# Kernel tuning notes

Hardware: AMD Instinct MI355X
Metric: run time of the kernel (lower is better)

The kernel has to match this reference:

```python
import jax, jax.numpy as jnp
import numpy as np

N = 50000       # nodes
E = 1_600_000   # edges (avg degree 32)
IN = 256        # in_dim
HID = 64        # hidden_dim
HEADS = 2
CLS = 10
NEG_SLOPE = 0.2  # PyG GATConv default leaky_relu slope


def gat_layer(x, edge_index, W, att_src, att_dst, bias, heads, concat):
    """PyG-style GATConv (eval mode, add_self_loops=True).
    x: [N, F_in]; W: [F_in, heads*C]; att_src/att_dst: [heads, C]; bias: [heads*C] or [C].
    """
    n = x.shape[0]
    loop = jnp.arange(n)
    src = jnp.concatenate([edge_index[0], loop])   # message sources j
    dst = jnp.concatenate([edge_index[1], loop])   # message targets i
    C = W.shape[1] // heads
    h = (x @ W).reshape(n, heads, C)               # [N, H, C]
    a_s = jnp.sum(h * att_src, axis=-1)            # [N, H]
    a_d = jnp.sum(h * att_dst, axis=-1)            # [N, H]
    e = jax.nn.leaky_relu(a_s[src] + a_d[dst], NEG_SLOPE)   # [E', H]
    # segment softmax over incoming edges of each destination node
    m = jax.lax.stop_gradient(jax.ops.segment_max(e, dst, num_segments=n))
    ex = jnp.exp(e - m[dst])
    denom = jax.ops.segment_sum(ex, dst, num_segments=n)
    alpha = ex / denom[dst]                         # [E', H]
    out = jax.ops.segment_sum(alpha[:, :, None] * h[src], dst, num_segments=n)  # [N, H, C]
    out = out.reshape(n, heads * C) if concat else out.mean(axis=1)
    return out + bias


def setup_inputs() -> dict:
    key = jax.random.key(0)
    ks = jax.random.split(key, 12)
    sd = lambda f: np.float32(1.0 / np.sqrt(f))
    x = jax.random.normal(ks[0], (N, IN), dtype=jnp.float32)
    edge_index = jax.random.randint(ks[1], (2, E), 0, N, dtype=jnp.int64)
    # layer 1: in_dim -> hidden, heads=2, concat
    W1 = jax.random.normal(ks[2], (IN, HEADS * HID), dtype=jnp.float32) * sd(IN)
    as1 = jax.random.normal(ks[3], (HEADS, HID), dtype=jnp.float32) * sd(HID)
    ad1 = jax.random.normal(ks[4], (HEADS, HID), dtype=jnp.float32) * sd(HID)
    b1 = jnp.zeros((HEADS * HID,), dtype=jnp.float32)
    # layer 2: hidden*heads -> hidden, heads=1, concat=False
    W2 = jax.random.normal(ks[5], (HEADS * HID, HID), dtype=jnp.float32) * sd(HEADS * HID)
    as2 = jax.random.normal(ks[6], (1, HID), dtype=jnp.float32) * sd(HID)
    ad2 = jax.random.normal(ks[7], (1, HID), dtype=jnp.float32) * sd(HID)
    b2 = jnp.zeros((HID,), dtype=jnp.float32)
    # linear head
    Wl = jax.random.normal(ks[8], (HID, CLS), dtype=jnp.float32) * sd(HID)
    bl = jnp.zeros((CLS,), dtype=jnp.float32)
    return {"x": x, "edge_index": edge_index,
            "W1": W1, "as1": as1, "ad1": ad1, "b1": b1,
            "W2": W2, "as2": as2, "ad2": ad2, "b2": b2,
            "Wl": Wl, "bl": bl}


def reference(x, edge_index, W1, as1, ad1, b1, W2, as2, ad2, b2, Wl, bl):
    h = jax.nn.elu(gat_layer(x, edge_index, W1, as1, ad1, b1, HEADS, True))
    h = jax.nn.elu(gat_layer(h, edge_index, W2, as2, ad2, b2, 1, False))
    return h @ Wl + bl  # [N, num_classes]
```

## Files before the change

### kernel.cpp

```cpp
#include <hip/hip_runtime.h>

#define NN 50000
#define NE 1600000
#define EP (NE + NN)
#define IN_DIM 256
#define HIDD 64
#define NCLS 10
#define NBKT 196
#define EPB 2048
#define NPB ((EP + EPB - 1) / EPB)
#define BCAP 12288

typedef unsigned short u16;
typedef short bf16x8 __attribute__((ext_vector_type(8)));
typedef float f32x4 __attribute__((ext_vector_type(4)));

__device__ __forceinline__ float b2f(u16 v) { return __uint_as_float(((unsigned)v) << 16); }
__device__ __forceinline__ u16 f2b(float f) {
    unsigned u = __float_as_uint(f);
    unsigned r = (u + 0x7FFFu + ((u >> 16) & 1u)) >> 16;
    return (u16)r;
}

__device__ __forceinline__ void load_edge(const int* __restrict__ ei, int m, int g,
                                          int& s, int& d) {
    if (g < NE) {
        if (m) { s = ei[2 * (size_t)g]; d = ei[2 * ((size_t)NE + g)]; }
        else   { s = ei[g];             d = ei[NE + g]; }
    } else {
        s = d = g - NE;
    }
    s = s < 0 ? 0 : (s >= NN ? NN - 1 : s);
    d = d < 0 ? 0 : (d >= NN ? NN - 1 : d);
}

__device__ __forceinline__ void wcvt_att_job(
    const float* __restrict__ W, const float* __restrict__ as,
    const float* __restrict__ ad, int K, int N, int H, u16* __restrict__ Wt,
    int idx) {
    if (idx >= K * (N + 16)) return;
    int n = idx / K, k = idx - n * K;
    if (n < N) { Wt[idx] = f2b(W[(size_t)k * N + n]); return; }
    int j = n - N;
    if (j >= 2 * H) { Wt[idx] = 0; return; }
    const float* att = (j & 1) ? ad : as;
    int h = j >> 1, C = N / H;
    float sum = 0.f;
    for (int c = 0; c < C; ++c)
        sum += W[(size_t)k * N + h * C + c] * att[h * C + c];
    Wt[idx] = f2b(sum);
}

__global__ __launch_bounds__(256) void wcvt_k(
    const float* __restrict__ W1, const float* __restrict__ as1,
    const float* __restrict__ ad1, u16* __restrict__ w1t,
    const float* __restrict__ W2, const float* __restrict__ as2,
    const float* __restrict__ ad2, u16* __restrict__ w2t,
    const float* __restrict__ Wl, u16* __restrict__ wlt,
    int* __restrict__ gcursor) {
    int b = blockIdx.x, t = threadIdx.x;
    if (b < 144) wcvt_att_job(W1, as1, ad1, 256, 128, 2, w1t, b * 256 + t);
    else if (b < 184) wcvt_att_job(W2, as2, ad2, 128, 64, 1, w2t, (b - 144) * 256 + t);
    else if (b < 188) {
        int idx = (b - 184) * 256 + t;
        int n = idx >> 6, k = idx & 63;
        wlt[n * 64 + k] = (n < NCLS) ? f2b(Wl[k * NCLS + n]) : (u16)0;
    } else {
        if (t < NBKT) gcursor[t] = 0;
    }
}

__device__ void partition_body(int b, const int* __restrict__ ei,
                               int* __restrict__ gcursor,
                               unsigned* __restrict__ bbuf) {
    __shared__ int hist[NBKT], base[NBKT], lbase[NBKT], lcur[NBKT];
    __shared__ int psc[256];
    __shared__ unsigned sst[EPB];
    __shared__ int smode;
    int t = threadIdx.x;
    if (t < 64) {
        int nz = 0;
#pragma unroll
        for (int k = 0; k < 4; ++k)
            if (ei[2 * (t * 4 + k) + 1] != 0) nz = 1;
        unsigned long long bal = __ballot(nz);
        if (t == 0) smode = (bal == 0ULL) ? 1 : 0;
    }
    for (int i = t; i < NBKT; i += 256) hist[i] = 0;
    __syncthreads();
    int m = smode;
    int g0 = b * EPB, gend = min(g0 + EPB, EP);
    unsigned ed[8];
#pragma unroll
    for (int i = 0; i < 4; ++i) {
        int g = g0 + i * 512 + 2 * t;
        int s0 = 0, d0 = 0, s1 = 0, d1 = 0;
        bool v0 = g < gend, v1 = g + 1 < gend;
        if (v1 && g >= NE) {
            s0 = d0 = g - NE; s1 = d1 = g + 1 - NE;
        } else if (v1 && g + 1 < NE) {
            if (m) {
                int4 sv = *(const int4*)(ei + 2 * (size_t)g);
                int4 dv = *(const int4*)(ei + 2 * ((size_t)NE + g));
                s0 = sv.x; s1 = sv.z; d0 = dv.x; d1 = dv.z;
            } else {
                int2 sv = *(const int2*)(ei + g);
                int2 dv = *(const int2*)(ei + NE + g);
                s0 = sv.x; s1 = sv.y; d0 = dv.x; d1 = dv.y;
            }
            s0 = s0 < 0 ? 0 : (s0 >= NN ? NN - 1 : s0);
            d0 = d0 < 0 ? 0 : (d0 >= NN ? NN - 1 : d0);
            s1 = s1 < 0 ? 0 : (s1 >= NN ? NN - 1 : s1);
            d1 = d1 < 0 ? 0 : (d1 >= NN ? NN - 1 : d1);
        } else {
            if (v0) load_edge(ei, m, g, s0, d0);
            if (v1) load_edge(ei, m, g + 1, s1, d1);
        }
        if (v0) { ed[2 * i] = ((unsigned)s0 << 16) | (unsigned)d0; atomicAdd(&hist[d0 >> 8], 1); }
        else ed[2 * i] = 0xFFFFFFFFu;
        if (v1) { ed[2 * i + 1] = ((unsigned)s1 << 16) | (unsigned)d1; atomicAdd(&hist[d1 >> 8], 1); }
        else ed[2 * i + 1] = 0xFFFFFFFFu;
    }
    __syncthreads();
    int hv = (t < NBKT) ? hist[t] : 0;
    psc[t] = hv;
    __syncthreads();
    for (int off = 1; off < 256; off <<= 1) {
        int x = (t >= off) ? psc[t - off] : 0;
        __syncthreads();
        psc[t] += x;
        __syncthreads();
    }
    if (t < NBKT) {
        lbase[t] = psc[t] - hv;
        lcur[t] = 0;
        base[t] = hv ? atomicAdd(&gcursor[t], hv) : 0;
    }
    __syncthreads();
#pragma unroll
    for (int i = 0; i < 8; ++i) {
        unsigned p = ed[i];
        if (p != 0xFFFFFFFFu) {
            int bb = (p & 0xFFFF) >> 8;
            int r = lbase[bb] + atomicAdd(&lcur[bb], 1);
            sst[r] = p;
        }
    }
    __syncthreads();
    int cnt = gend - g0;
    for (int l = t; l < cnt; l += 256) {
        unsigned p = sst[l];
        int bb = (p & 0xFFFF) >> 8;
        int gp = base[bb] + (l - lbase[bb]);
        if (gp < BCAP)
            bbuf[(size_t)bb * BCAP + gp] = ((p >> 16) << 8) | (p & 255u);
    }
}

template <int K, int NF, int H, bool F32A, bool SLICED_A, bool SLICED_C>
__device__ __forceinline__ void gemm_body(
    int bb, const float* __restrict__ Af, const u16* __restrict__ Ab,
    const u16* __restrict__ Wt, u16* __restrict__ C,
    float* __restrict__ a_s, float* __restrict__ a_d) {
    constexpr int NTF = NF / 16, NT = NTF + 1, KS = K / 32;
    const int wave = threadIdx.x >> 6, lane = threadIdx.x & 63;
    const int quad = lane >> 4, l15 = lane & 15;
    const int m0 = bb * 64 + wave * 16;
    int rowA = m0 + l15;
    if (rowA >= NN) rowA = NN - 1;
    const float* afp = F32A ? (Af + (size_t)rowA * K + quad * 8) : nullptr;
    const u16* abp = nullptr;
    if constexpr (!F32A) {
        abp = SLICED_A ? (Ab + (size_t)rowA * 32 + quad * 8)
                       : (Ab + (size_t)rowA * K + quad * 8);
    }
    const u16* bptr = Wt + (size_t)l15 * K + quad * 8;
    f32x4 acc[NT] = {};
#pragma unroll
    for (int ks = 0; ks < KS; ++ks) {
        bf16x8 af;
        if constexpr (F32A) {
            float4 v0 = *(const float4*)(afp + ks * 32);
            float4 v1 = *(const float4*)(afp + ks * 32 + 4);
            af[0] = (short)f2b(v0.x); af[1] = (short)f2b(v0.y);
            af[2] = (short)f2b(v0.z); af[3] = (short)f2b(v0.w);
            af[4] = (short)f2b(v1.x); af[5] = (short)f2b(v1.y);
            af[6] = (short)f2b(v1.z); af[7] = (short)f2b(v1.w);
        } else {
            af = SLICED_A ? *(const bf16x8*)(abp + (size_t)ks * (NN * 32))
                          : *(const bf16x8*)(abp + ks * 32);
        }
        bf16x8 bf[NT];
#pragma unroll
        for (int nt = 0; nt < NT; ++nt)
            bf[nt] = *(const bf16x8*)(bptr + (size_t)nt * 16 * K + ks * 32);
#pragma unroll
        for (int nt = 0; nt < NT; ++nt)
            acc[nt] = __builtin_amdgcn_mfma_f32_16x16x32_bf16(af, bf[nt], acc[nt], 0, 0, 0);
    }
#pragma unroll
    for (int nt = 0; nt < NTF; ++nt) {
#pragma unroll
        for (int reg = 0; reg < 4; ++reg) {
            int row = m0 + quad * 4 + reg;
            int c = nt * 16 + l15;
            if (row < NN) {
                if constexpr (SLICED_C)
                    C[(size_t)(c >> 5) * (NN * 32) + (size_t)row * 32 + (c & 31)] =
                        f2b(acc[nt][reg]);
                else
                    C[(size_t)row * NF + c] = f2b(acc[nt][reg]);
            }
        }
    }
    if (l15 < 2 * H) {
        int h = l15 >> 1;
        float* dst = (l15 & 1) ? a_d : a_s;
#pragma unroll
        for (int reg = 0; reg < 4; ++reg) {
            int row = m0 + quad * 4 + reg;
            if (row < NN) dst[row * H + h] = acc[NTF][reg];
        }
    }
}

__global__ __launch_bounds__(256) void part_gemm_k(
    const int* __restrict__ ei, int* __restrict__ gcursor,
    unsigned* __restrict__ bbuf, const float* __restrict__ x,
    const u16* __restrict__ w1t, u16* __restrict__ hb,
    float* __restrict__ a_s, float* __restrict__ a_d) {
    if (blockIdx.x < NPB)
        partition_body(blockIdx.x, ei, gcursor, bbuf);
    else
        gemm_body<256, 128, 2, true, false, false>(blockIdx.x - NPB, x, nullptr,
                                                   w1t, hb, a_s, a_d);
}

__global__ __launch_bounds__(256) void gemm2_k(
    const u16* __restrict__ Ab, const u16* __restrict__ Wt, u16* __restrict__ C,
    float* __restrict__ a_s, float* __restrict__ a_d) {
    gemm_body<128, 64, 1, false, true, true>(blockIdx.x, nullptr, Ab, Wt, C, a_s, a_d);
}

__global__ __launch_bounds__(1024) void bucket_csr_k(const unsigned* __restrict__ bbuf,
                                                     const int* __restrict__ gcursor,
                                                     int* __restrict__ row_ptr,
                                                     u16* __restrict__ csr_src) {
    __shared__ int bsc[256];
    __shared__ int hist[256], scn[256], cur[256];
    __shared__ int se0, scnt, stot;
    __shared__ u16 srt[BCAP];
    int b = blockIdx.x, t = threadIdx.x;
    int v = 0;
    if (t < 256) {
        v = (t < NBKT) ? min(gcursor[t], BCAP) : 0;
        bsc[t] = v;
        hist[t] = 0;
    }
    __syncthreads();
    for (int off = 1; off < 256; off <<= 1) {
        int x = (t < 256 && t >= off) ? bsc[t - off] : 0;
        __syncthreads();
        if (t < 256) bsc[t] += x;
        __syncthreads();
    }
    if (t == b) { se0 = bsc[t] - v; scnt = v; }
    if (t == NBKT - 1) stot = bsc[t];
    __syncthreads();
    int e0 = se0, cnt = scnt;
    const unsigned* bb = bbuf + (size_t)b * BCAP;
    for (int e = t; e < cnt; e += 1024)
        atomicAdd(&hist[bb[e] & 255], 1);
    __syncthreads();
    int hv = 0;
    if (t < 256) { hv = hist[t]; scn[t] = hv; }
    __syncthreads();
    for (int off = 1; off < 256; off <<= 1) {
        int x = (t < 256 && t >= off) ? scn[t - off] : 0;
        __syncthreads();
        if (t < 256) scn[t] += x;
        __syncthreads();
    }
    if (t < 256) {
        int ex = scn[t] - hv;
        int n = b * 256 + t;
        if (n < NN) row_ptr[n] = e0 + ex;
        cur[t] = ex;
    }
    __syncthreads();
    for (int e = t; e < cnt; e += 1024) {
        unsigned p = bb[e];
        int pos = atomicAdd(&cur[p & 255], 1);
        srt[pos] = (u16)(p >> 8);
    }
    __syncthreads();
    for (int e = t; e < cnt; e += 1024)
        csr_src[e0 + e] = srt[e];
    if (b == 0 && t == 0) row_ptr[NN] = stot;
}

template <int CH, int H, bool HEAD>
__global__ __launch_bounds__(256) void gat_gather_k(
    const int* __restrict__ row_ptr, const u16* __restrict__ csr_src,
    const float* __restrict__ a_s, const float* __restrict__ a_d,
    const u16* __restrict__ h, const float* __restrict__ bias,
    u16* __restrict__ outg, const float* __restrict__ Wl,
    const float* __restrict__ bl, float* __restrict__ outh) {
    constexpr int VEC = CH / 64;
    constexpr int JB = 16;
    int n = (blockIdx.x * blockDim.x + threadIdx.x) >> 6;
    int lane = threadIdx.x & 63;
    if (n >= NN) return;
    int r0 = row_ptr[n], r1 = row_ptr[n + 1];
    const bool hi = (VEC == 2) ? (lane >= 32) : false;
    const int shl16 = hi ? 0 : 16;

    float adn0, adn1 = 0.f;
    if (H == 2) {
        float2 adv = *(const float2*)(a_d + n * 2);
        adn0 = adv.x; adn1 = adv.y;
    } else {
        adn0 = a_d[n];
    }

    float dh0 = 0.f, dh1 = 0.f;
    float acc[VEC];
#pragma unroll
    for (int v = 0; v < VEC; ++v) acc[v] = 0.f;

    for (int base = r0; base < r1; base += 64) {
        int cnt = min(64, r1 - base);
        int idx = base + lane;
        bool act = idx < r1;
        int sl = act ? (int)csr_src[idx] : 0;
        unsigned pex;
        if (H == 2) {
            float2 av = *(const float2*)(a_s + sl * 2);
            float e0 = av.x + adn0;
            e0 = e0 > 0.f ? e0 : 0.2f * e0;
            e0 = fminf(e0, 60.f);
            float ex0 = act ? __expf(e0) : 0.f;
            dh0 += ex0;
            float e1 = av.y + adn1;
            e1 = e1 > 0.f ? e1 : 0.2f * e1;
            e1 = fminf(e1, 60.f);
            float ex1 = act ? __expf(e1) : 0.f;
            dh1 += ex1;
            pex = (unsigned)f2b(ex0) | ((unsigned)f2b(ex1) << 16);
        } else {
            float e0 = a_s[sl] + adn0;
            e0 = e0 > 0.f ? e0 : 0.2f * e0;
            e0 = fminf(e0, 60.f);
            float ex0 = act ? __expf(e0) : 0.f;
            dh0 += ex0;
            pex = (unsigned)sl | ((unsigned)f2b(ex0) << 16);
        }
        for (int j0 = 0; j0 < cnt; j0 += JB) {
            if (VEC == 2) {
                int ssu[JB];
                unsigned peu[JB];
#pragma unroll
                for (int i = 0; i < JB; ++i) {
                    ssu[i] = __builtin_amdgcn_readlane(sl, j0 + i);
                    peu[i] = (unsigned)__builtin_amdgcn_readlane((int)pex, j0 + i);
                }
                unsigned hv[JB];
#pragma unroll
                for (int i = 0; i < JB; ++i)
                    hv[i] = ((const unsigned*)(h + (size_t)ssu[i] * CH))[lane];
#pragma unroll
                for (int i = 0; i < JB; ++i) {
                    float exv = __uint_as_float((peu[i] << shl16) & 0xFFFF0000u);
                    acc[0] += exv * __uint_as_float(hv[i] << 16);
                    acc[1] += exv * __uint_as_float(hv[i] & 0xFFFF0000u);
                }
            } else {
                unsigned peu[JB];
#pragma unroll
                for (int i = 0; i < JB; ++i)
                    peu[i] = (unsigned)__builtin_amdgcn_readlane((int)pex, j0 + i);
                u16 hv[JB];
#pragma unroll
                for (int i = 0; i < JB; ++i)
                    hv[i] = (h + (size_t)(peu[i] & 0xFFFFu) * CH)[lane];
#pragma unroll
                for (int i = 0; i < JB; ++i)
                    acc[0] += __uint_as_float(peu[i] & 0xFFFF0000u) * b2f(hv[i]);
            }
        }
    }

#pragma unroll
    for (int off = 32; off; off >>= 1) dh0 += __shfl_xor(dh0, off);
    float dn = dh0;
    if (H == 2) {
#pragma unroll
        for (int off = 32; off; off >>= 1) dh1 += __shfl_xor(dh1, off);
        dn = hi ? dh1 : dh0;
    }

    if (VEC == 2) {
        int c = lane * 2;
        float2 bv = *(const float2*)(bias + c);
        float v0 = acc[0] / dn + bv.x;
        float v1 = acc[1] / dn + bv.y;
        v0 = v0 > 0.f ? v0 : expm1f(v0);
        v1 = v1 > 0.f ? v1 : expm1f(v1);
        ushort2 ov;
        ov.x = f2b(v0); ov.y = f2b(v1);
        *(ushort2*)(outg + (size_t)(c >> 5) * (NN * 32) + (size_t)n * 32 + (c & 31)) = ov;
    } else {
        float v0 = acc[0] / dn + bias[lane];
        v0 = v0 > 0.f ? v0 : expm1f(v0);
        if (HEAD) {
#pragma unroll
            for (int cls = 0; cls < NCLS; ++cls) {
                float p = v0 * Wl[lane * NCLS + cls];
#pragma unroll
                for (int off = 32; off; off >>= 1) p += __shfl_xor(p, off);
                if (lane == cls) outh[(size_t)n * NCLS + cls] = p + bl[cls];
            }
        } else {
            outg[(size_t)n * CH + lane] = f2b(v0);
        }
    }
}

__global__ __launch_bounds__(256) void edge_alpha_k(
    const int* __restrict__ row_ptr, const u16* __restrict__ csr_src,
    const float* __restrict__ a_s, const float* __restrict__ a_d,
    unsigned* __restrict__ A2, float* __restrict__ dninv) {
    int wave = threadIdx.x >> 6;
    int pair = blockIdx.x * 4 + wave;
    if (pair >= NN / 2) return;
    int lane = threadIdx.x & 63, half = lane >> 5, hl = lane & 31;
    int node = pair * 2 + half;
    int r0 = row_ptr[node], r1 = row_ptr[node + 1];
    int cnt = r1 - r0;
    int co = max(cnt, __shfl_xor(cnt, 32));
    int nbat = (co + 31) >> 5;
    float adn = a_d[node];
    float dh = 0.f;
    for (int b = 0; b < nbat; ++b) {
        int idx = r0 + b * 32 + hl;
        bool act = idx < r1;
        int sl = act ? (int)csr_src[idx] : 0;
        float e = a_s[sl] + adn;
        e = e > 0.f ? e : 0.2f * e;
        e = fminf(e, 60.f);
        float ex = act ? __expf(e) : 0.f;
        dh += ex;
        if (act)
            __builtin_nontemporal_store(
                (unsigned)sl | ((unsigned)f2b(ex) << 16), A2 + idx);
    }
#pragma unroll
    for (int off = 1; off < 32; off <<= 1) dh += __shfl_xor(dh, off);
    if (hl == 0) dninv[node] = 1.0f / dh;
}

template <int CH, int NSL, int H, bool USE_EX>
__global__ __launch_bounds__(256) void gat_slice_k(
    const int* __restrict__ row_ptr, const u16* __restrict__ csr_src,
    const unsigned* __restrict__ A2, const float* __restrict__ a_s,
    const float* __restrict__ a_d, const float* __restrict__ dninv,
    const u16* __restrict__ h, const float* __restrict__ bias,
    u16* __restrict__ outg) {
    constexpr int SC = CH / NSL;
    constexpr int SUB = 8 / NSL;
    int xcd = blockIdx.x & 7;
    int slice = xcd / SUB;
    int sub = xcd % SUB;
    int pg = (blockIdx.x >> 3) * SUB + sub;
    int wave = threadIdx.x >> 6;
    int pair = pg * 4 + wave;
    if (pair >= NN / 2) return;
    int lane = threadIdx.x & 63;
    int half = lane >> 5, hl = lane & 31, q = hl & 7, gh = hl >> 3;
    int node = pair * 2 + half;
    int r0 = row_ptr[node], r1 = row_ptr[node + 1];
    int cnt = r1 - r0;
    int co = max(cnt, __shfl_xor(cnt, 32));
    int nbat = (co + 31) >> 5;
    const unsigned char* hb8 =
        (const unsigned char*)h + (size_t)slice * (NN * 64);
    const int head = (H == 2) ? (slice >> 1) : 0;
    float adn = 0.f, rdn = 0.f;
    if constexpr (USE_EX) rdn = dninv[node];
    else adn = a_d[node * H + head];
    float dh = 0.f;
    float acc[4] = {0.f, 0.f, 0.f, 0.f};
    const int abase = ((half << 5) | gh) << 2;
    for (int b = 0; b < nbat; ++b) {
        int idx = r0 + b * 32 + hl;
        bool act = idx < r1;
        unsigned pex;
        if constexpr (USE_EX) {
            pex = act ? __builtin_nontemporal_load(A2 + idx) : 0u;
        } else {
            int sl = act ? (int)__builtin_nontemporal_load(csr_src + idx) : 0;
            float e = a_s[sl * H + head] + adn;
            e = e > 0.f ? e : 0.2f * e;
            e = fminf(e, 60.f);
            float ex = act ? __expf(e) : 0.f;
            dh += ex;
            pex = (unsigned)sl | ((unsigned)f2b(ex) << 16);
        }
#pragma unroll
        for (int jr = 0; jr < 2; ++jr) {
            int pr[4];
#pragma unroll
            for (int i = 0; i < 4; ++i)
                pr[i] = __builtin_amdgcn_ds_bpermute(
                    abase + ((jr * 16 + i * 4) << 2), (int)pex);
            unsigned hv0[4], hv1[4];
#pragma unroll
            for (int i = 0; i < 4; ++i) {
                const unsigned* p = (const unsigned*)(
                    hb8 + (((unsigned)((unsigned)pr[i] & 0xFFFFu) << 6) + q * 8));
                hv0[i] = p[0];
                hv1[i] = p[1];
            }
#pragma unroll
            for (int i = 0; i < 4; ++i) {
                float exf = __uint_as_float((unsigned)pr[i] & 0xFFFF0000u);
                unsigned w0 = hv0[i], w1 = hv1[i];
                acc[0] += exf * __uint_as_float(w0 << 16);
                acc[1] += exf * __uint_as_float(w0 & 0xFFFF0000u);
                acc[2] += exf * __uint_as_float(w1 << 16);
                acc[3] += exf * __uint_as_float(w1 & 0xFFFF0000u);
            }
        }
    }
    if constexpr (!USE_EX) {
#pragma unroll
        for (int off = 1; off < 32; off <<= 1) dh += __shfl_xor(dh, off);
        rdn = 1.0f / dh;
    }
#pragma unroll
    for (int v = 0; v < 4; ++v) {
        acc[v] += __shfl_xor(acc[v], 8);
        acc[v] += __shfl_xor(acc[v], 16);
    }
    if (gh == 0) {
        float vv[4];
#pragma unroll
        for (int k = 0; k < 4; ++k) {
            float t = acc[k] * rdn + bias[slice * SC + q * 4 + k];
            vv[k] = t > 0.f ? t : expm1f(t);
        }
        unsigned long long ov =
            (unsigned long long)((unsigned)f2b(vv[0]) | ((unsigned)f2b(vv[1]) << 16)) |
            ((unsigned long long)((unsigned)f2b(vv[2]) | ((unsigned)f2b(vv[3]) << 16)) << 32);
        __builtin_nontemporal_store(
            ov, (unsigned long long*)(outg + (size_t)slice * (NN * 32) +
                                      (size_t)node * 32 + q * 4));
    }
}

__global__ __launch_bounds__(256) void head_gemm_k(
    const u16* __restrict__ A, const u16* __restrict__ Wt,
    const float* __restrict__ bl, float* __restrict__ out) {
    const int wave = threadIdx.x >> 6, lane = threadIdx.x & 63;
    const int quad = lane >> 4, l15 = lane & 15;
    const int m0 = blockIdx.x * 64 + wave * 16;
    int rowA = m0 + l15;
    if (rowA >= NN) rowA = NN - 1;
    const u16* ab = A + (size_t)rowA * 32 + quad * 8;
    const u16* bp = Wt + (size_t)l15 * 64 + quad * 8;
    f32x4 acc = {};
#pragma unroll
    for (int ks = 0; ks < 2; ++ks) {
        bf16x8 af = *(const bf16x8*)(ab + (size_t)ks * (NN * 32));
        bf16x8 bf = *(const bf16x8*)(bp + ks * 32);
        acc = __builtin_amdgcn_mfma_f32_16x16x32_bf16(af, bf, acc, 0, 0, 0);
    }
    if (l15 < NCLS) {
        float blv = bl[l15];
#pragma unroll
        for (int reg = 0; reg < 4; ++reg) {
            int row = m0 + quad * 4 + reg;
            if (row < NN) out[(size_t)row * NCLS + l15] = acc[reg] + blv;
        }
    }
}

extern "C" void kernel_launch(void* const* d_in, const int* in_sizes, int n_in,
                              void* d_out, int out_size, void* d_ws, size_t ws_size,
                              hipStream_t stream) {
    const float* x   = (const float*)d_in[0];
    const int*   ei  = (const int*)d_in[1];
    const float* W1  = (const float*)d_in[2];
    const float* as1 = (const float*)d_in[3];
    const float* ad1 = (const float*)d_in[4];
    const float* b1  = (const float*)d_in[5];
    const float* W2  = (const float*)d_in[6];
    const float* as2 = (const float*)d_in[7];
    const float* ad2 = (const float*)d_in[8];
    const float* b2  = (const float*)d_in[9];
    const float* Wl  = (const float*)d_in[10];
    const float* bl  = (const float*)d_in[11];
    float* out = (float*)d_out;

    float* ws = (float*)d_ws;
    size_t o = 0;
    u16* hb  = (u16*)(ws + o); o += (size_t)NN * 64;
    u16* g2  = hb + (size_t)NN * 64;
    u16* g1  = (u16*)(ws + o); o += (size_t)NN * 64;
    unsigned* bbuf = (unsigned*)g1;
    unsigned* A2 = (unsigned*)g1;
    float* dn2inv = (float*)((char*)g1 + (size_t)EP * 4);
    u16* w1t = (u16*)(ws + o); o += 144 * 256 / 2;
    u16* w2t = (u16*)(ws + o); o += 80 * 128 / 2;
    u16* wlt = (u16*)(ws + o); o += 16 * 64 / 2;
    float* a_s = ws + o;       o += (size_t)NN * 2;
    float* a_d = ws + o;       o += (size_t)NN * 2;
    int* ints = (int*)(ws + o);
    size_t io = 0;
    int* gcursor  = ints + io; io += NBKT;
    int* row_ptr  = ints + io; io += NN + 1;
    u16* csr_src  = (u16*)(ints + io); io += (EP + 1) / 2;

    const int gemmBlocks = (NN + 63) / 64;
    const int gatherBlocks = (NN + 3) / 4;

    wcvt_k<<<189, 256, 0, stream>>>(W1, as1, ad1, w1t, W2, as2, ad2, w2t,
                                    Wl, wlt, gcursor);
    part_gemm_k<<<NPB + gemmBlocks, 256, 0, stream>>>(
        ei, gcursor, bbuf, x, w1t, hb, a_s, a_d);
    bucket_csr_k<<<NBKT, 1024, 0, stream>>>(bbuf, gcursor, row_ptr, csr_src);
    gat_gather_k<128, 2, false><<<gatherBlocks, 256, 0, stream>>>(
        row_ptr, csr_src, a_s, a_d, hb, b1, g1, nullptr, nullptr, nullptr);
    gemm2_k<<<gemmBlocks, 256, 0, stream>>>(g1, w2t, hb, a_s, a_d);
    edge_alpha_k<<<(NN / 2 + 3) / 4, 256, 0, stream>>>(
        row_ptr, csr_src, a_s, a_d, A2, dn2inv);
    gat_slice_k<64, 2, 1, true><<<12504, 256, 0, stream>>>(
        row_ptr, csr_src, A2, nullptr, nullptr, dn2inv, hb, b2, g2);
    head_gemm_k<<<gemmBlocks, 256, 0, stream>>>(g2, wlt, bl, out);
}
```

Baseline: 305.8 us.

## Fuse layer-2 aggregation with linear head into one wave-per-node kernel

```diff
diff --git a/kernel.cpp b/kernel.cpp
--- a/kernel.cpp
+++ b/kernel.cpp
@@ -56,16 +56,11 @@
     const float* __restrict__ ad1, u16* __restrict__ w1t,
     const float* __restrict__ W2, const float* __restrict__ as2,
     const float* __restrict__ ad2, u16* __restrict__ w2t,
-    const float* __restrict__ Wl, u16* __restrict__ wlt,
     int* __restrict__ gcursor) {
     int b = blockIdx.x, t = threadIdx.x;
     if (b < 144) wcvt_att_job(W1, as1, ad1, 256, 128, 2, w1t, b * 256 + t);
     else if (b < 184) wcvt_att_job(W2, as2, ad2, 128, 64, 1, w2t, (b - 144) * 256 + t);
-    else if (b < 188) {
-        int idx = (b - 184) * 256 + t;
-        int n = idx >> 6, k = idx & 63;
-        wlt[n * 64 + k] = (n < NCLS) ? f2b(Wl[k * NCLS + n]) : (u16)0;
-    } else {
+    else {
         if (t < NBKT) gcursor[t] = 0;
     }
 }
@@ -239,7 +234,7 @@
 __global__ __launch_bounds__(256) void gemm2_k(
     const u16* __restrict__ Ab, const u16* __restrict__ Wt, u16* __restrict__ C,
     float* __restrict__ a_s, float* __restrict__ a_d) {
-    gemm_body<128, 64, 1, false, true, true>(blockIdx.x, nullptr, Ab, Wt, C, a_s, a_d);
+    gemm_body<128, 64, 1, false, true, false>(blockIdx.x, nullptr, Ab, Wt, C, a_s, a_d);
 }
 
 __global__ __launch_bounds__(1024) void bucket_csr_k(const unsigned* __restrict__ bbuf,
@@ -412,17 +407,7 @@
     } else {
         float v0 = acc[0] / dn + bias[lane];
         v0 = v0 > 0.f ? v0 : expm1f(v0);
-        if (HEAD) {
-#pragma unroll
-            for (int cls = 0; cls < NCLS; ++cls) {
-                float p = v0 * Wl[lane * NCLS + cls];
-#pragma unroll
-                for (int off = 32; off; off >>= 1) p += __shfl_xor(p, off);
-                if (lane == cls) outh[(size_t)n * NCLS + cls] = p + bl[cls];
-            }
-        } else {
-            outg[(size_t)n * CH + lane] = f2b(v0);
-        }
+        outg[(size_t)n * CH + lane] = f2b(v0);
     }
 }
 
@@ -459,129 +444,65 @@
     if (hl == 0) dninv[node] = 1.0f / dh;
 }
 
-template <int CH, int NSL, int H, bool USE_EX>
-__global__ __launch_bounds__(256) void gat_slice_k(
-    const int* __restrict__ row_ptr, const u16* __restrict__ csr_src,
-    const unsigned* __restrict__ A2, const float* __restrict__ a_s,
-    const float* __restrict__ a_d, const float* __restrict__ dninv,
-    const u16* __restrict__ h, const float* __restrict__ bias,
-    u16* __restrict__ outg) {
-    constexpr int SC = CH / NSL;
-    constexpr int SUB = 8 / NSL;
-    int xcd = blockIdx.x & 7;
-    int slice = xcd / SUB;
-    int sub = xcd % SUB;
-    int pg = (blockIdx.x >> 3) * SUB + sub;
-    int wave = threadIdx.x >> 6;
-    int pair = pg * 4 + wave;
-    if (pair >= NN / 2) return;
+__global__ __launch_bounds__(256) void gat2_head_k(
+    const int* __restrict__ row_ptr, const unsigned* __restrict__ A2,
+    const float* __restrict__ dninv, const u16* __restrict__ h,
+    const float* __restrict__ bias, const float* __restrict__ Wl,
+    const float* __restrict__ bl, float* __restrict__ out) {
+    int n = (blockIdx.x * blockDim.x + threadIdx.x) >> 6;
     int lane = threadIdx.x & 63;
-    int half = lane >> 5, hl = lane & 31, q = hl & 7, gh = hl >> 3;
-    int node = pair * 2 + half;
-    int r0 = row_ptr[node], r1 = row_ptr[node + 1];
-    int cnt = r1 - r0;
-    int co = max(cnt, __shfl_xor(cnt, 32));
-    int nbat = (co + 31) >> 5;
-    const unsigned char* hb8 =
-        (const unsigned char*)h + (size_t)slice * (NN * 64);
-    const int head = (H == 2) ? (slice >> 1) : 0;
-    float adn = 0.f, rdn = 0.f;
-    if constexpr (USE_EX) rdn = dninv[node];
-    else adn = a_d[node * H + head];
-    float dh = 0.f;
-    float acc[4] = {0.f, 0.f, 0.f, 0.f};
-    const int abase = ((half << 5) | gh) << 2;
-    for (int b = 0; b < nbat; ++b) {
-        int idx = r0 + b * 32 + hl;
-        bool act = idx < r1;
-        unsigned pex;
-        if constexpr (USE_EX) {
-            pex = act ? __builtin_nontemporal_load(A2 + idx) : 0u;
-        } else {
-            int sl = act ? (int)__builtin_nontemporal_load(csr_src + idx) : 0;
-            float e = a_s[sl * H + head] + adn;
-            e = e > 0.f ? e : 0.2f * e;
-            e = fminf(e, 60.f);
-            float ex = act ? __expf(e) : 0.f;
-            dh += ex;
-            pex = (unsigned)sl | ((unsigned)f2b(ex) << 16);
-        }
-#pragma unroll
-        for (int jr = 0; jr < 2; ++jr) {
-            int pr[4];
-#pragma unroll
-            for (int i = 0; i < 4; ++i)
-                pr[i] = __builtin_amdgcn_ds_bpermute(
-                    abase + ((jr * 16 + i * 4) << 2), (int)pex);
-            unsigned hv0[4], hv1[4];
-#pragma unroll
-            for (int i = 0; i < 4; ++i) {
-                const unsigned* p = (const unsigned*)(
-                    hb8 + (((unsigned)((unsigned)pr[i] & 0xFFFFu) << 6) + q * 8));
-                hv0[i] = p[0];
-                hv1[i] = p[1];
-            }
-#pragma unroll
-            for (int i = 0; i < 4; ++i) {
-                float exf = __uint_as_float((unsigned)pr[i] & 0xFFFF0000u);
-                unsigned w0 = hv0[i], w1 = hv1[i];
-                acc[0] += exf * __uint_as_float(w0 << 16);
-                acc[1] += exf * __uint_as_float(w0 & 0xFFFF0000u);
-                acc[2] += exf * __uint_as_float(w1 << 16);
-                acc[3] += exf * __uint_as_float(w1 & 0xFFFF0000u);
-            }
-        }
-    }
-    if constexpr (!USE_EX) {
-#pragma unroll
-        for (int off = 1; off < 32; off <<= 1) dh += __shfl_xor(dh, off);
-        rdn = 1.0f / dh;
-    }
-#pragma unroll
-    for (int v = 0; v < 4; ++v) {
+    if (n >= NN) return;
+    int r0 = row_ptr[n], r1 = row_ptr[n + 1];
+    int q = lane & 7, g = lane >> 3;
+    float rdn = dninv[n];
+    float acc[8];
+#pragma unroll
+    for (int v = 0; v < 8; ++v) acc[v] = 0.f;
+
+    for (int base = r0; base < r1; base += 64) {
+        int cnt = min(64, r1 - base);
+        int idx = base + lane;
+        unsigned pex = (idx < r1) ? __builtin_nontemporal_load(A2 + idx) : 0u;
+        for (int j0 = 0; j0 < cnt; j0 += 8) {
+            int pr = __builtin_amdgcn_ds_bpermute((j0 + g) << 2, (int)pex);
+            float exf = __uint_as_float((unsigned)pr & 0xFFFF0000u);
+            const unsigned* p = (const unsigned*)(
+                h + (size_t)((unsigned)pr & 0xFFFFu) * 64 + q * 8);
+            unsigned w0 = p[0], w1 = p[1], w2 = p[2], w3 = p[3];
+            acc[0] += exf * __uint_as_float(w0 << 16);
+            acc[1] += exf * __uint_as_float(w0 & 0xFFFF0000u);
+            acc[2] += exf * __uint_as_float(w1 << 16);
+            acc[3] += exf * __uint_as_float(w1 & 0xFFFF0000u);
+            acc[4] += exf * __uint_as_float(w2 << 16);
+            acc[5] += exf * __uint_as_float(w2 & 0xFFFF0000u);
+            acc[6] += exf * __uint_as_float(w3 << 16);
+            acc[7] += exf * __uint_as_float(w3 & 0xFFFF0000u);
+        }
+    }
+#pragma unroll
+    for (int v = 0; v < 8; ++v) {
         acc[v] += __shfl_xor(acc[v], 8);
         acc[v] += __shfl_xor(acc[v], 16);
-    }
-    if (gh == 0) {
-        float vv[4];
-#pragma unroll
-        for (int k = 0; k < 4; ++k) {
-            float t = acc[k] * rdn + bias[slice * SC + q * 4 + k];
-            vv[k] = t > 0.f ? t : expm1f(t);
-        }
-        unsigned long long ov =
-            (unsigned long long)((unsigned)f2b(vv[0]) | ((unsigned)f2b(vv[1]) << 16)) |
-            ((unsigned long long)((unsigned)f2b(vv[2]) | ((unsigned)f2b(vv[3]) << 16)) << 32);
-        __builtin_nontemporal_store(
-            ov, (unsigned long long*)(outg + (size_t)slice * (NN * 32) +
-                                      (size_t)node * 32 + q * 4));
-    }
-}
-
-__global__ __launch_bounds__(256) void head_gemm_k(
-    const u16* __restrict__ A, const u16* __restrict__ Wt,
-    const float* __restrict__ bl, float* __restrict__ out) {
-    const int wave = threadIdx.x >> 6, lane = threadIdx.x & 63;
-    const int quad = lane >> 4, l15 = lane & 15;
-    const int m0 = blockIdx.x * 64 + wave * 16;
-    int rowA = m0 + l15;
-    if (rowA >= NN) rowA = NN - 1;
-    const u16* ab = A + (size_t)rowA * 32 + quad * 8;
-    const u16* bp = Wt + (size_t)l15 * 64 + quad * 8;
-    f32x4 acc = {};
-#pragma unroll
-    for (int ks = 0; ks < 2; ++ks) {
-        bf16x8 af = *(const bf16x8*)(ab + (size_t)ks * (NN * 32));
-        bf16x8 bf = *(const bf16x8*)(bp + ks * 32);
-        acc = __builtin_amdgcn_mfma_f32_16x16x32_bf16(af, bf, acc, 0, 0, 0);
-    }
-    if (l15 < NCLS) {
-        float blv = bl[l15];
-#pragma unroll
-        for (int reg = 0; reg < 4; ++reg) {
-            int row = m0 + quad * 4 + reg;
-            if (row < NN) out[(size_t)row * NCLS + l15] = acc[reg] + blv;
-        }
+        acc[v] += __shfl_xor(acc[v], 32);
+    }
+    float t01 = (lane & 8) ? acc[1] : acc[0];
+    float t23 = (lane & 8) ? acc[3] : acc[2];
+    float t45 = (lane & 8) ? acc[5] : acc[4];
+    float t67 = (lane & 8) ? acc[7] : acc[6];
+    float ta = (lane & 16) ? t23 : t01;
+    float tb = (lane & 16) ? t67 : t45;
+    float ts = (lane & 32) ? tb : ta;
+    int srcl = ((lane & 7) << 3) | (lane >> 3);
+    float vsw = __uint_as_float(
+        __builtin_amdgcn_ds_bpermute(srcl << 2, __float_as_int(ts)));
+    float v0 = vsw * rdn + bias[lane];
+    v0 = v0 > 0.f ? v0 : expm1f(v0);
+#pragma unroll
+    for (int cls = 0; cls < NCLS; ++cls) {
+        float p = v0 * Wl[lane * NCLS + cls];
+#pragma unroll
+        for (int off = 32; off; off >>= 1) p += __shfl_xor(p, off);
+        if (lane == cls) out[(size_t)n * NCLS + cls] = p + bl[cls];
     }
 }
 
@@ -605,14 +526,12 @@
     float* ws = (float*)d_ws;
     size_t o = 0;
     u16* hb  = (u16*)(ws + o); o += (size_t)NN * 64;
-    u16* g2  = hb + (size_t)NN * 64;
     u16* g1  = (u16*)(ws + o); o += (size_t)NN * 64;
     unsigned* bbuf = (unsigned*)g1;
     unsigned* A2 = (unsigned*)g1;
     float* dn2inv = (float*)((char*)g1 + (size_t)EP * 4);
     u16* w1t = (u16*)(ws + o); o += 144 * 256 / 2;
     u16* w2t = (u16*)(ws + o); o += 80 * 128 / 2;
-    u16* wlt = (u16*)(ws + o); o += 16 * 64 / 2;
     float* a_s = ws + o;       o += (size_t)NN * 2;
     float* a_d = ws + o;       o += (size_t)NN * 2;
     int* ints = (int*)(ws + o);
@@ -624,8 +543,7 @@
     const int gemmBlocks = (NN + 63) / 64;
     const int gatherBlocks = (NN + 3) / 4;
 
-    wcvt_k<<<189, 256, 0, stream>>>(W1, as1, ad1, w1t, W2, as2, ad2, w2t,
-                                    Wl, wlt, gcursor);
+    wcvt_k<<<185, 256, 0, stream>>>(W1, as1, ad1, w1t, W2, as2, ad2, w2t, gcursor);
     part_gemm_k<<<NPB + gemmBlocks, 256, 0, stream>>>(
         ei, gcursor, bbuf, x, w1t, hb, a_s, a_d);
     bucket_csr_k<<<NBKT, 1024, 0, stream>>>(bbuf, gcursor, row_ptr, csr_src);
@@ -634,7 +552,6 @@
     gemm2_k<<<gemmBlocks, 256, 0, stream>>>(g1, w2t, hb, a_s, a_d);
     edge_alpha_k<<<(NN / 2 + 3) / 4, 256, 0, stream>>>(
         row_ptr, csr_src, a_s, a_d, A2, dn2inv);
-    gat_slice_k<64, 2, 1, true><<<12504, 256, 0, stream>>>(
-        row_ptr, csr_src, A2, nullptr, nullptr, dn2inv, hb, b2, g2);
-    head_gemm_k<<<gemmBlocks, 256, 0, stream>>>(g2, wlt, bl, out);
-}
+    gat2_head_k<<<gatherBlocks, 256, 0, stream>>>(
+        row_ptr, A2, dn2inv, hb, b2, Wl, bl, out);
+}
```

Result: slower. 320.0 us (+4.6%).

## Split bucket CSR build into four sub-bucket blocks per bucket

Applied to the files above, without the earlier changes.

```diff
diff --git a/kernel.cpp b/kernel.cpp
--- a/kernel.cpp
+++ b/kernel.cpp
@@ -10,6 +10,8 @@
 #define EPB 2048
 #define NPB ((EP + EPB - 1) / EPB)
 #define BCAP 12288
+#define QS 4
+#define QCAP 3072
 
 typedef unsigned short u16;
 typedef short bf16x8 __attribute__((ext_vector_type(8)));
@@ -247,16 +249,18 @@
                                                      int* __restrict__ row_ptr,
                                                      u16* __restrict__ csr_src) {
     __shared__ int bsc[256];
-    __shared__ int hist[256], scn[256], cur[256];
+    __shared__ int hist[64], scn[64], cur[64];
+    __shared__ int qcnt[QS];
     __shared__ int se0, scnt, stot;
-    __shared__ u16 srt[BCAP];
-    int b = blockIdx.x, t = threadIdx.x;
+    __shared__ u16 srt[QCAP];
+    int blk = blockIdx.x, b = blk >> 2, q = blk & 3, t = threadIdx.x;
     int v = 0;
     if (t < 256) {
         v = (t < NBKT) ? min(gcursor[t], BCAP) : 0;
         bsc[t] = v;
-        hist[t] = 0;
-    }
+    }
+    if (t < 64) hist[t] = 0;
+    if (t < QS) qcnt[t] = 0;
     __syncthreads();
     for (int off = 1; off < 256; off <<= 1) {
         int x = (t < 256 && t >= off) ? bsc[t - off] : 0;
@@ -267,36 +271,60 @@
     if (t == b) { se0 = bsc[t] - v; scnt = v; }
     if (t == NBKT - 1) stot = bsc[t];
     __syncthreads();
-    int e0 = se0, cnt = scnt;
+    int cnt = scnt;
     const unsigned* bb = bbuf + (size_t)b * BCAP;
-    for (int e = t; e < cnt; e += 1024)
-        atomicAdd(&hist[bb[e] & 255], 1);
-    __syncthreads();
-    int hv = 0;
-    if (t < 256) { hv = hist[t]; scn[t] = hv; }
-    __syncthreads();
-    for (int off = 1; off < 256; off <<= 1) {
-        int x = (t < 256 && t >= off) ? scn[t - off] : 0;
-        __syncthreads();
-        if (t < 256) scn[t] += x;
-        __syncthreads();
-    }
-    if (t < 256) {
-        int ex = scn[t] - hv;
-        int n = b * 256 + t;
-        if (n < NN) row_ptr[n] = e0 + ex;
-        cur[t] = ex;
-    }
-    __syncthreads();
+    int c0 = 0, c1 = 0, c2 = 0, c3 = 0;
     for (int e = t; e < cnt; e += 1024) {
         unsigned p = bb[e];
-        int pos = atomicAdd(&cur[p & 255], 1);
-        srt[pos] = (u16)(p >> 8);
-    }
-    __syncthreads();
-    for (int e = t; e < cnt; e += 1024)
-        csr_src[e0 + e] = srt[e];
-    if (b == 0 && t == 0) row_ptr[NN] = stot;
+        int loc = p & 255;
+        int qq = loc >> 6;
+        c0 += (qq == 0); c1 += (qq == 1); c2 += (qq == 2); c3 += (qq == 3);
+        if (qq == q) atomicAdd(&hist[loc & 63], 1);
+    }
+#pragma unroll
+    for (int off = 32; off; off >>= 1) {
+        c0 += __shfl_xor(c0, off); c1 += __shfl_xor(c1, off);
+        c2 += __shfl_xor(c2, off); c3 += __shfl_xor(c3, off);
+    }
+    if ((t & 63) == 0) {
+        if (c0) atomicAdd(&qcnt[0], c0);
+        if (c1) atomicAdd(&qcnt[1], c1);
+        if (c2) atomicAdd(&qcnt[2], c2);
+        if (c3) atomicAdd(&qcnt[3], c3);
+    }
+    __syncthreads();
+    int e0q = se0 + (q > 0 ? qcnt[0] : 0) + (q > 1 ? qcnt[1] : 0) +
+              (q > 2 ? qcnt[2] : 0);
+    int myc = qcnt[q];
+    int hv = 0;
+    if (t < 64) { hv = hist[t]; scn[t] = hv; }
+    __syncthreads();
+    for (int off = 1; off < 64; off <<= 1) {
+        int x = (t < 64 && t >= off) ? scn[t - off] : 0;
+        __syncthreads();
+        if (t < 64) scn[t] += x;
+        __syncthreads();
+    }
+    if (t < 64) {
+        int ex = scn[t] - hv;
+        int n = b * 256 + q * 64 + t;
+        if (n < NN) row_ptr[n] = e0q + ex;
+        cur[t] = ex;
+    }
+    __syncthreads();
+    for (int e = t; e < cnt; e += 1024) {
+        unsigned p = bb[e];
+        int loc = p & 255;
+        if ((loc >> 6) == q) {
+            int pos = atomicAdd(&cur[loc & 63], 1);
+            if (pos < QCAP) srt[pos] = (u16)(p >> 8);
+        }
+    }
+    __syncthreads();
+    int wn = min(myc, QCAP);
+    for (int e = t; e < wn; e += 1024)
+        csr_src[e0q + e] = srt[e];
+    if (blk == 0 && t == 0) row_ptr[NN] = stot;
 }
 
 template <int CH, int H, bool HEAD>
@@ -412,17 +440,7 @@
     } else {
         float v0 = acc[0] / dn + bias[lane];
         v0 = v0 > 0.f ? v0 : expm1f(v0);
-        if (HEAD) {
-#pragma unroll
-            for (int cls = 0; cls < NCLS; ++cls) {
-                float p = v0 * Wl[lane * NCLS + cls];
-#pragma unroll
-                for (int off = 32; off; off >>= 1) p += __shfl_xor(p, off);
-                if (lane == cls) outh[(size_t)n * NCLS + cls] = p + bl[cls];
-            }
-        } else {
-            outg[(size_t)n * CH + lane] = f2b(v0);
-        }
+        outg[(size_t)n * CH + lane] = f2b(v0);
     }
 }
 
@@ -628,7 +646,7 @@
                                     Wl, wlt, gcursor);
     part_gemm_k<<<NPB + gemmBlocks, 256, 0, stream>>>(
         ei, gcursor, bbuf, x, w1t, hb, a_s, a_d);
-    bucket_csr_k<<<NBKT, 1024, 0, stream>>>(bbuf, gcursor, row_ptr, csr_src);
+    bucket_csr_k<<<NBKT * QS, 1024, 0, stream>>>(bbuf, gcursor, row_ptr, csr_src);
     gat_gather_k<128, 2, false><<<gatherBlocks, 256, 0, stream>>>(
         row_ptr, csr_src, a_s, a_d, hb, b1, g1, nullptr, nullptr, nullptr);
     gemm2_k<<<gemmBlocks, 256, 0, stream>>>(g1, w2t, hb, a_s, a_d);
```

New measurement: 319.0 us. 1.04x slower.
